# Kernel tuning notes

Hardware: AMD Instinct MI355X
Metric: run time of the kernel (lower is better)

The kernel has to match this reference:

```python
import jax, jax.numpy as jnp
import numpy as np

N = 2048          # num_points
H = 128
W = 128
T = 2             # frames
DEG = 2           # polynomial degree (coeff rows = DEG + 1)


def setup_inputs() -> dict:
    key = jax.random.key(0)
    k1, k2, k3, k4, k5, k6 = jax.random.split(key, 6)
    # xyz: c0 = atanh(2*(rand-0.5)) as in __init__ (keep away from +-1), higher orders small
    u = jax.random.uniform(k1, (N, 2), minval=0.02, maxval=0.98)
    xyz_c0 = jnp.arctanh(2.0 * (u - 0.5))
    xyz_hi = 0.1 * jax.random.normal(k2, (DEG, N, 2))
    xyz_coeffs = jnp.concatenate([xyz_c0[None], xyz_hi], axis=0).astype(jnp.float32)
    # cholesky: c0 = [1,0,1] + 0.01*randn, higher orders small
    chol_c0 = jnp.array([1.0, 0.0, 1.0])[None, :] + 0.01 * jax.random.normal(k3, (N, 3))
    chol_hi = 0.05 * jax.random.normal(k4, (DEG, N, 3))
    cholesky_coeffs = jnp.concatenate([chol_c0[None], chol_hi], axis=0).astype(jnp.float32)
    # opacity coeffs (c0 zeros in __init__, use small noise for non-trivial grads)
    opacity_coeffs = (0.5 * jax.random.normal(k5, (DEG + 1, N, 1))).astype(jnp.float32)
    features_dc = jax.random.normal(k6, (N, 3)).astype(jnp.float32)
    t_values = jnp.linspace(0.0, 1.0, T).astype(jnp.float32)
    return {
        "xyz_coeffs": xyz_coeffs,
        "cholesky_coeffs": cholesky_coeffs,
        "opacity_coeffs": opacity_coeffs,
        "features_dc": features_dc,
        "t_values": t_values,
    }


def _forward(xyz_coeffs, cholesky_coeffs, opacity_coeffs, features_dc, t_values):
    deg_p1 = xyz_coeffs.shape[0]
    # t_power_matrix: [T, deg+1]
    tp = t_values[:, None] ** jnp.arange(deg_p1, dtype=t_values.dtype)[None, :]
    # polynomial trajectories
    xy = jnp.tanh(jnp.einsum("td,dnc->tnc", tp, xyz_coeffs))            # [T,N,2] in (-1,1)
    mx = 0.5 * (xy[..., 0] + 1.0) * W                                    # [T,N] pixel x
    my = 0.5 * (xy[..., 1] + 1.0) * H                                    # [T,N] pixel y
    chol = jnp.einsum("td,dnk->tnk", tp, cholesky_coeffs)
    chol = chol + jnp.array([0.5, 0.0, 0.5], dtype=chol.dtype)           # cholesky bound
    l0, l1, l2 = chol[..., 0], chol[..., 1], chol[..., 2]
    # Sigma = L L^T with L = [[l0,0],[l1,l2]]
    s11 = l0 * l0
    s12 = l0 * l1
    s22 = l1 * l1 + l2 * l2
    det = s11 * s22 - s12 * s12
    ca = s22 / det                                                       # conic a
    cb = -s12 / det                                                      # conic b
    cc = s11 / det                                                       # conic c
    opac = jax.nn.sigmoid(jnp.einsum("td,dnk->tnk", tp, opacity_coeffs))[..., 0]  # [T,N]
    colors = jax.nn.sigmoid(features_dc)                                 # [N,3]
    px = jnp.arange(W, dtype=mx.dtype) + 0.5                             # pixel centers
    py = jnp.arange(H, dtype=mx.dtype) + 0.5

    def render_frame(mx_t, my_t, a_t, b_t, c_t, op_t):
        dx = mx_t[:, None] - px[None, :]                                 # [N,W]
        dy = my_t[:, None] - py[None, :]                                 # [N,H]
        # quadratic form per (n,h,w): a*dx^2 + 2*b*dx*dy + c*dy^2
        q = (a_t[:, None, None] * (dx * dx)[:, None, :]
             + 2.0 * b_t[:, None, None] * dy[:, :, None] * dx[:, None, :]
             + c_t[:, None, None] * (dy * dy)[:, :, None])               # [N,H,W]
        wgt = jnp.exp(-0.5 * q) * op_t[:, None, None]                    # [N,H,W]
        return jnp.einsum("nhw,nc->chw", wgt, colors)                    # [3,H,W]

    imgs = jax.vmap(render_frame)(mx, my, ca, cb, cc, opac)              # [T,3,H,W]
    return jnp.clip(imgs, 0.0, 1.0)


def reference(xyz_coeffs, cholesky_coeffs, opacity_coeffs, features_dc, t_values):
    return _forward(xyz_coeffs, cholesky_coeffs, opacity_coeffs, features_dc, t_values)
```

## Files before the change

### kernel.cpp

```cpp
#include <hip/hip_runtime.h>

#define N_PTS  2048
#define T_FR   2
#define IMG    128
#define HW     (IMG * IMG)
#define BLOCK  512
#define WAVES  8
#define SEG    256
#define QCUT   36.043653f

#if defined(__has_builtin)
#if __has_builtin(__builtin_amdgcn_exp2f)
#define FAST_EXP2(x) __builtin_amdgcn_exp2f(x)
#endif
#endif
#ifndef FAST_EXP2
#define FAST_EXP2(x) exp2f(x)
#endif

__device__ __forceinline__ float sigmoid_fast(float x) {
    return 1.0f / (1.0f + FAST_EXP2(-1.44269504089f * x));
}
__device__ __forceinline__ float tanh_fast(float x) {
    return 1.0f - 2.0f / (FAST_EXP2(2.88539008178f * x) + 1.0f);
}

__launch_bounds__(BLOCK, 4)
__global__ void gi_fused(const float* __restrict__ xyz,
                         const float* __restrict__ chol,
                         const float* __restrict__ opa,
                         const float* __restrict__ feat,
                         const float* __restrict__ tv,
                         float* __restrict__ out) {
    __shared__ float4 sA[WAVES][SEG];
    __shared__ float4 sB[WAVES][SEG];
    __shared__ int    sCnt[WAVES];
    __shared__ float  red[BLOCK * 3];

    const int bid  = blockIdx.x;
    const int t    = bid >> 8;
    const int tile = bid & 255;
    const int h0   = (tile >> 4) << 3;
    const int w0   = (tile & 15) << 3;
    const int tid  = threadIdx.x;
    const int lane = tid & 63;
    const int wv   = tid >> 6;

    const float tt = tv[t];
    const float t2 = tt * tt;
    const float K  = -0.72134752044f;
    const float cx = (float)w0 + 4.0f;
    const float cy = (float)h0 + 4.0f;

    int cnt = 0;
#pragma unroll 4
    for (int j = 0; j < SEG / 64; ++j) {
        const int g = wv * SEG + j * 64 + lane;

        const float2 x0 = *(const float2*)&xyz[g * 2];
        const float2 x1 = *(const float2*)&xyz[N_PTS * 2 + g * 2];
        const float2 x2 = *(const float2*)&xyz[2 * N_PTS * 2 + g * 2];
        float mx = 64.0f * (tanh_fast(fmaf(t2, x2.x, fmaf(tt, x1.x, x0.x))) + 1.0f);
        float my = 64.0f * (tanh_fast(fmaf(t2, x2.y, fmaf(tt, x1.y, x0.y))) + 1.0f);

        float l0 = fmaf(t2, chol[2 * N_PTS * 3 + g * 3 + 0],
                   fmaf(tt, chol[N_PTS * 3 + g * 3 + 0], chol[g * 3 + 0])) + 0.5f;
        float l1 = fmaf(t2, chol[2 * N_PTS * 3 + g * 3 + 1],
                   fmaf(tt, chol[N_PTS * 3 + g * 3 + 1], chol[g * 3 + 1]));
        float l2 = fmaf(t2, chol[2 * N_PTS * 3 + g * 3 + 2],
                   fmaf(tt, chol[N_PTS * 3 + g * 3 + 2], chol[g * 3 + 2])) + 0.5f;

        float s11 = l0 * l0;
        float s12 = l0 * l1;
        float s22 = fmaf(l1, l1, l2 * l2);

        bool hit = (fabsf(mx - cx) <= sqrtf(QCUT * s11) + 3.5f) &&
                   (fabsf(my - cy) <= sqrtf(QCUT * s22) + 3.5f);
        unsigned long long m = __ballot(hit);
        if (hit) {
            float det  = fmaf(s11, s22, -s12 * s12);
            float Kinv = K / det;
            float po = fmaf(t2, opa[2 * N_PTS + g], fmaf(tt, opa[N_PTS + g], opa[g]));
            float op = sigmoid_fast(po);
            int pos = cnt + (int)__popcll(m & ((1ull << lane) - 1ull));
            sA[wv][pos] = make_float4(mx, my, s22 * Kinv, -2.0f * s12 * Kinv);
            sB[wv][pos] = make_float4(s11 * Kinv,
                                      op * sigmoid_fast(feat[g * 3 + 0]),
                                      op * sigmoid_fast(feat[g * 3 + 1]),
                                      op * sigmoid_fast(feat[g * 3 + 2]));
        }
        cnt += (int)__popcll(m);
    }
    if (lane == 0) sCnt[wv] = cnt;
    __syncthreads();

    const float px = (float)(w0 + (lane & 7)) + 0.5f;
    const float py = (float)(h0 + (lane >> 3)) + 0.5f;
    const int   L  = sCnt[wv];

    float accr = 0.0f, accg = 0.0f, accb = 0.0f;
    for (int i = 0; i < L; ++i) {
        float4 A = sA[wv][i];
        float4 B = sB[wv][i];
        float dx = A.x - px;
        float dy = A.y - py;
        float t1 = fmaf(A.w, dy, A.z * dx);
        float q  = fmaf(B.x * dy, dy, t1 * dx);
        float wgt = FAST_EXP2(q);
        accr = fmaf(wgt, B.y, accr);
        accg = fmaf(wgt, B.z, accg);
        accb = fmaf(wgt, B.w, accb);
    }

    red[tid * 3 + 0] = accr;
    red[tid * 3 + 1] = accg;
    red[tid * 3 + 2] = accb;
    __syncthreads();

    if (tid < 64) {
        float rr = 0.0f, gg = 0.0f, bb = 0.0f;
#pragma unroll
        for (int w8 = 0; w8 < WAVES; ++w8) {
            rr += red[(w8 * 64 + tid) * 3 + 0];
            gg += red[(w8 * 64 + tid) * 3 + 1];
            bb += red[(w8 * 64 + tid) * 3 + 2];
        }
        const int h   = h0 + (tid >> 3);
        const int w   = w0 + (tid & 7);
        const int pix = h * IMG + w;
        out[(t * 3 + 0) * HW + pix] = fminf(fmaxf(rr, 0.0f), 1.0f);
        out[(t * 3 + 1) * HW + pix] = fminf(fmaxf(gg, 0.0f), 1.0f);
        out[(t * 3 + 2) * HW + pix] = fminf(fmaxf(bb, 0.0f), 1.0f);
    }
}

extern "C" void kernel_launch(void* const* d_in, const int* in_sizes, int n_in,
                              void* d_out, int out_size, void* d_ws, size_t ws_size,
                              hipStream_t stream) {
    const float* xyz  = (const float*)d_in[0];
    const float* chol = (const float*)d_in[1];
    const float* opa  = (const float*)d_in[2];
    const float* feat = (const float*)d_in[3];
    const float* tv   = (const float*)d_in[4];

    gi_fused<<<T_FR * 256, BLOCK, 0, stream>>>(
        xyz, chol, opa, feat, tv, (float*)d_out);
}
```

Baseline: 13.83 us.

## Broadcast culled Gaussians via readlane instead of LDS compaction

Replaces the per-wave LDS staging of culled Gaussian parameters and the intermediate barrier with direct register broadcasts. Each hit lane's parameters go to the whole wave with readlane, iterating over the ballot mask. This removes LDS writes and reads, one __syncthreads, and most of the shared memory footprint, which may raise occupancy. In exchange each splat now costs eight readlane scalar operations plus loop-carried bit scanning, and the per-chunk loops are fully unrolled.

New measurement: 15.01 us. +8.5%, slower.

```diff
diff --git a/kernel.cpp b/kernel.cpp
--- a/kernel.cpp
+++ b/kernel.cpp
@@ -6,7 +6,7 @@
 #define HW     (IMG * IMG)
 #define BLOCK  512
 #define WAVES  8
-#define SEG    256
+#define SEG    (N_PTS / WAVES)
 #define QCUT   36.043653f
 
 #if defined(__has_builtin)
@@ -24,6 +24,9 @@
 __device__ __forceinline__ float tanh_fast(float x) {
     return 1.0f - 2.0f / (FAST_EXP2(2.88539008178f * x) + 1.0f);
 }
+__device__ __forceinline__ float rdlane(float v, int l) {
+    return __int_as_float(__builtin_amdgcn_readlane(__float_as_int(v), l));
+}
 
 __launch_bounds__(BLOCK, 4)
 __global__ void gi_fused(const float* __restrict__ xyz,
@@ -32,10 +35,7 @@
                          const float* __restrict__ feat,
                          const float* __restrict__ tv,
                          float* __restrict__ out) {
-    __shared__ float4 sA[WAVES][SEG];
-    __shared__ float4 sB[WAVES][SEG];
-    __shared__ int    sCnt[WAVES];
-    __shared__ float  red[BLOCK * 3];
+    __shared__ float red[BLOCK * 3];
 
     const int bid  = blockIdx.x;
     const int t    = bid >> 8;
@@ -51,9 +51,12 @@
     const float K  = -0.72134752044f;
     const float cx = (float)w0 + 4.0f;
     const float cy = (float)h0 + 4.0f;
+    const float px = (float)(w0 + (lane & 7)) + 0.5f;
+    const float py = (float)(h0 + (lane >> 3)) + 0.5f;
 
-    int cnt = 0;
-#pragma unroll 4
+    float accr = 0.0f, accg = 0.0f, accb = 0.0f;
+
+#pragma unroll
     for (int j = 0; j < SEG / 64; ++j) {
         const int g = wv * SEG + j * 64 + lane;
 
@@ -76,40 +79,37 @@
 
         bool hit = (fabsf(mx - cx) <= sqrtf(QCUT * s11) + 3.5f) &&
                    (fabsf(my - cy) <= sqrtf(QCUT * s22) + 3.5f);
-        unsigned long long m = __ballot(hit);
+
+        float pa = 0.0f, pb2 = 0.0f, pc = 0.0f, pr = 0.0f, pg = 0.0f, pb = 0.0f;
         if (hit) {
             float det  = fmaf(s11, s22, -s12 * s12);
             float Kinv = K / det;
+            pa  = s22 * Kinv;
+            pb2 = -2.0f * s12 * Kinv;
+            pc  = s11 * Kinv;
             float po = fmaf(t2, opa[2 * N_PTS + g], fmaf(tt, opa[N_PTS + g], opa[g]));
             float op = sigmoid_fast(po);
-            int pos = cnt + (int)__popcll(m & ((1ull << lane) - 1ull));
-            sA[wv][pos] = make_float4(mx, my, s22 * Kinv, -2.0f * s12 * Kinv);
-            sB[wv][pos] = make_float4(s11 * Kinv,
-                                      op * sigmoid_fast(feat[g * 3 + 0]),
-                                      op * sigmoid_fast(feat[g * 3 + 1]),
-                                      op * sigmoid_fast(feat[g * 3 + 2]));
+            pr = op * sigmoid_fast(feat[g * 3 + 0]);
+            pg = op * sigmoid_fast(feat[g * 3 + 1]);
+            pb = op * sigmoid_fast(feat[g * 3 + 2]);
         }
-        cnt += (int)__popcll(m);
-    }
-    if (lane == 0) sCnt[wv] = cnt;
-    __syncthreads();
 
-    const float px = (float)(w0 + (lane & 7)) + 0.5f;
-    const float py = (float)(h0 + (lane >> 3)) + 0.5f;
-    const int   L  = sCnt[wv];
-
-    float accr = 0.0f, accg = 0.0f, accb = 0.0f;
-    for (int i = 0; i < L; ++i) {
-        float4 A = sA[wv][i];
-        float4 B = sB[wv][i];
-        float dx = A.x - px;
-        float dy = A.y - py;
-        float t1 = fmaf(A.w, dy, A.z * dx);
-        float q  = fmaf(B.x * dy, dy, t1 * dx);
-        float wgt = FAST_EXP2(q);
-        accr = fmaf(wgt, B.y, accr);
-        accg = fmaf(wgt, B.z, accg);
-        accb = fmaf(wgt, B.w, accb);
+        unsigned long long m = __ballot(hit);
+        while (m) {
+            int l = __builtin_ctzll(m);
+            m &= m - 1ull;
+            float bmx = rdlane(mx, l),  bmy = rdlane(my, l);
+            float ba  = rdlane(pa, l),  bb2 = rdlane(pb2, l), bc = rdlane(pc, l);
+            float br  = rdlane(pr, l),  bg  = rdlane(pg, l),  bb = rdlane(pb, l);
+            float dx = bmx - px;
+            float dy = bmy - py;
+            float t1 = fmaf(ba, dx, bb2 * dy);
+            float q  = fmaf(bc * dy, dy, t1 * dx);
+            float wgt = FAST_EXP2(q);
+            accr = fmaf(wgt, br, accr);
+            accg = fmaf(wgt, bg, accg);
+            accb = fmaf(wgt, bb, accb);
+        }
     }
 
     red[tid * 3 + 0] = accr;
```
